# Kernel optimization log

Measured on AMD Instinct MI355X. Metric: run time of the kernel, lower is better.

The kernel has to match this reference:

```python
import jax, jax.numpy as jnp
import numpy as np

G, N, C_IN, C_OUT, HEADS = 64, 2048, 64, 64, 2
E = 1_000_000
T = G * N  # total flattened nodes
NEG_SLOPE = 0.2  # PyG GATv2Conv default


def setup_inputs() -> dict:
    key = jax.random.key(0)
    k_x, k_e, k_wl, k_wr, k_a, k_b = jax.random.split(key, 6)
    x = jax.random.normal(k_x, (G, N, C_IN), dtype=jnp.float32)
    edge_index = jax.random.randint(k_e, (2, E), 0, T, dtype=jnp.int64)
    # GATv2Conv params (share_weights=False): separate lin_l / lin_r, per-head att vector, bias
    s = 1.0 / np.sqrt(C_IN)
    W_l = jax.random.uniform(k_wl, (C_IN, HEADS * C_OUT), minval=-s, maxval=s, dtype=jnp.float32)
    W_r = jax.random.uniform(k_wr, (C_IN, HEADS * C_OUT), minval=-s, maxval=s, dtype=jnp.float32)
    att = jax.random.normal(k_a, (HEADS, C_OUT), dtype=jnp.float32) * 0.1
    bias = jax.random.normal(k_b, (HEADS * C_OUT,), dtype=jnp.float32) * 0.01
    return {"x": x, "edge_index": edge_index, "W_l": W_l, "W_r": W_r, "att": att, "bias": bias}


def reference(x, edge_index, W_l, W_r, att, bias):
    # Flatten batched nodes: (G, N, C_in) -> (T, C_in)
    x_flat = x.reshape(-1, C_IN)
    # Linear projections per side, split heads: (T, H, C)
    xl = (x_flat @ W_l).reshape(T, HEADS, C_OUT)
    xr = (x_flat @ W_r).reshape(T, HEADS, C_OUT)
    # add_self_loops=True: append (i, i) for every flattened node
    loop = jnp.arange(T, dtype=edge_index.dtype)
    src = jnp.concatenate([edge_index[0], loop])
    dst = jnp.concatenate([edge_index[1], loop])
    # GATv2 scoring: e_ij = att . LeakyReLU(xl[j] + xr[i])  -> (E', H)
    h = jax.nn.leaky_relu(xl[src] + xr[dst], negative_slope=NEG_SLOPE)
    score = jnp.einsum('ehc,hc->eh', h, att)
    # Segment softmax over incoming edges of each destination node
    m = jax.ops.segment_max(score, dst, num_segments=T)  # (T, H)
    ealpha = jnp.exp(score - m[dst])
    denom = jax.ops.segment_sum(ealpha, dst, num_segments=T)
    alpha = ealpha / denom[dst]  # self-loops guarantee denom > 0
    # Scatter-aggregate messages: out[i] = sum_j alpha_ij * xl[j]
    out = jax.ops.segment_sum(alpha[:, :, None] * xl[src], dst, num_segments=T)  # (T, H, C)
    out = out.reshape(T, HEADS * C_OUT) + bias
    return out.reshape(G, N, HEADS * C_OUT)
```

## Files before the change

### kernel.cpp

```cpp
#include <hip/hip_runtime.h>
#include <hip/hip_bf16.h>

#define T_NODES (64 * 2048)
#define CIN 64
#define HC 128
#define NEG_SLOPE 0.2f
#define GEMM_BLOCKS (T_NODES / 64)

typedef unsigned short ushort_t;
typedef __attribute__((ext_vector_type(8))) short bf16x8;
typedef __attribute__((ext_vector_type(4))) float f32x4;

__device__ __forceinline__ ushort_t f2bf(float x) {
    unsigned u = __float_as_uint(x);
    u += 0x7fffu + ((u >> 16) & 1u);
    return (ushort_t)(u >> 16);
}
__device__ __forceinline__ float bf2f(ushort_t b) {
    return __uint_as_float(((unsigned)b) << 16);
}

__global__ void prep_w(const float* __restrict__ Wl, const float* __restrict__ Wr,
                       uint4* __restrict__ wt) {
    const int t = blockIdx.x * 256 + threadIdx.x;
    const int n = t & 255, cc = t >> 8;
    const float* Wsrc = ((n < HC) ? Wl : Wr) + (n & (HC - 1));
    union { ushort_t u[8]; uint4 v; } pk;
#pragma unroll
    for (int j = 0; j < 8; ++j) pk.u[j] = f2bf(Wsrc[(cc * 8 + j) * HC]);
    const int sw = (n & 7) << 4;
    *(uint4*)((char*)wt + n * 128 + ((cc * 16) ^ sw)) = pk.v;
}

__global__ __launch_bounds__(256) void gemm_hist(const float* __restrict__ x,
                                                 const uint4* __restrict__ wt,
                                                 ushort_t* __restrict__ xl,
                                                 ushort_t* __restrict__ xr,
                                                 const int* __restrict__ ei,
                                                 unsigned* __restrict__ counts,
                                                 ushort_t* __restrict__ rank,
                                                 int E, int ET, int histBlocks) {
    __shared__ uint4 lds4[2560];
    const int tid = threadIdx.x;

    if (blockIdx.x < histBlocks) {
        const int b = blockIdx.x;
#pragma unroll
        for (int e = 0; e < 4; ++e) {
            int i = b * 1024 + e * 256 + tid;
            if (i < ET) {
                int dst = (i < E) ? ei[E + i] : (i - E);
                rank[i] = (ushort_t)atomicAdd(&counts[dst], 1u);
            }
        }
        return;
    }

    char* abase = (char*)lds4;
    char* wbase = (char*)lds4 + 8192;
    const int row0 = (blockIdx.x - histBlocks) * 64;

    {
        const int r = tid >> 2, c4 = tid & 3;
        const float4* xp = (const float4*)(x + (size_t)(row0 + r) * CIN + c4 * 16);
        float4 f0 = xp[0], f1 = xp[1], f2 = xp[2], f3 = xp[3];
        union { ushort_t u[16]; uint4 v[2]; } pk;
        const float s[16] = {f0.x,f0.y,f0.z,f0.w, f1.x,f1.y,f1.z,f1.w,
                             f2.x,f2.y,f2.z,f2.w, f3.x,f3.y,f3.z,f3.w};
#pragma unroll
        for (int j = 0; j < 16; ++j) pk.u[j] = f2bf(s[j]);
        const int sw = (r & 7) << 4;
        *(uint4*)(abase + r * 128 + ((c4 * 32)      ^ sw)) = pk.v[0];
        *(uint4*)(abase + r * 128 + ((c4 * 32 + 16) ^ sw)) = pk.v[1];
    }
    {
#pragma unroll
        for (int q = 0; q < 8; ++q)
            lds4[512 + q * 256 + tid] = wt[q * 256 + tid];
    }
    __syncthreads();

    const int wave = tid >> 6;
    const int lane = tid & 63;
    const int ar = lane & 15;
    const int kb = lane >> 4;

    bf16x8 afr[2][4], bfr[2][4];
#pragma unroll
    for (int kk = 0; kk < 2; ++kk) {
#pragma unroll
        for (int rt = 0; rt < 4; ++rt) {
            const int r = rt * 16 + ar;
            afr[kk][rt] = *(bf16x8*)(abase + r * 128 + ((kk * 64 + kb * 16) ^ ((r & 7) << 4)));
        }
#pragma unroll
        for (int ct = 0; ct < 4; ++ct) {
            const int n = wave * 64 + ct * 16 + ar;
            bfr[kk][ct] = *(bf16x8*)(wbase + n * 128 + ((kk * 64 + kb * 16) ^ ((n & 7) << 4)));
        }
    }

    f32x4 acc[4][4];
#pragma unroll
    for (int rt = 0; rt < 4; ++rt)
#pragma unroll
        for (int ct = 0; ct < 4; ++ct) acc[rt][ct] = (f32x4){0.f, 0.f, 0.f, 0.f};

#pragma unroll
    for (int kk = 0; kk < 2; ++kk)
#pragma unroll
        for (int rt = 0; rt < 4; ++rt)
#pragma unroll
            for (int ct = 0; ct < 4; ++ct)
                acc[rt][ct] = __builtin_amdgcn_mfma_f32_16x16x32_bf16(
                    afr[kk][rt], bfr[kk][ct], acc[rt][ct], 0, 0, 0);

    ushort_t* op = (wave < 2) ? xl : xr;
    const int colbase = (wave & 1) * 64 + ar;
    const int rowoff = (lane >> 4) * 4;
#pragma unroll
    for (int rt = 0; rt < 4; ++rt)
#pragma unroll
        for (int ct = 0; ct < 4; ++ct)
#pragma unroll
            for (int j = 0; j < 4; ++j)
                op[(size_t)(row0 + rt * 16 + rowoff + j) * HC + colbase + ct * 16] =
                    f2bf(acc[rt][ct][j]);
}

__global__ __launch_bounds__(256) void scan_tiles(const unsigned* __restrict__ counts,
                                                  unsigned* __restrict__ offs,
                                                  unsigned* __restrict__ partials) {
    __shared__ unsigned s[256];
    const int t = threadIdx.x;
    const int base = blockIdx.x * 1024 + t * 4;
    uint4 c = *(const uint4*)(counts + base);
    unsigned mysum = c.x + c.y + c.z + c.w;
    s[t] = mysum;
    __syncthreads();
    for (int off = 1; off < 256; off <<= 1) {
        unsigned v = (t >= off) ? s[t - off] : 0u;
        __syncthreads();
        s[t] += v;
        __syncthreads();
    }
    unsigned excl = s[t] - mysum;
    uint4 o;
    o.x = excl;
    o.y = excl + c.x;
    o.z = o.y + c.y;
    o.w = o.z + c.z;
    *(uint4*)(offs + base) = o;
    if (t == 255) partials[blockIdx.x] = s[255];
}

__global__ __launch_bounds__(256) void finalize_offs(unsigned* __restrict__ offs,
                                                     const unsigned* __restrict__ partials) {
    __shared__ unsigned s[128];
    const int t = threadIdx.x;
    const int tile = blockIdx.x >> 2;
    if (t < 128) s[t] = (t < tile) ? partials[t] : 0u;
    __syncthreads();
    for (int off = 64; off; off >>= 1) {
        if (t < off) s[t] += s[t + off];
        __syncthreads();
    }
    const unsigned base = s[0];
    const int i = blockIdx.x * 256 + t;
    offs[i] += base;
}

__global__ void scatter_edges(const int* __restrict__ ei,
                              const unsigned* __restrict__ offs,
                              const ushort_t* __restrict__ rank,
                              int* __restrict__ sorted_src, int E, int ET) {
    int i = blockIdx.x * 256 + threadIdx.x;
    if (i >= ET) return;
    int src, dst;
    if (i < E) { src = ei[i]; dst = ei[E + i]; }
    else       { src = dst = i - E; }
    sorted_src[offs[dst] + rank[i]] = src;
}

__global__ __launch_bounds__(256) void fused_aggr(const ushort_t* __restrict__ xl,
                                                  const ushort_t* __restrict__ xr,
                                                  const int* __restrict__ sorted_src,
                                                  const unsigned* __restrict__ offs,
                                                  const unsigned* __restrict__ counts,
                                                  const float* __restrict__ att,
                                                  const float* __restrict__ bias,
                                                  float* __restrict__ out) {
    const int tid = threadIdx.x;
    const int lane = tid & 63;
    int node = (blockIdx.x * 256 + tid) >> 6;
    node = __builtin_amdgcn_readfirstlane(node);
    const int slot = lane >> 4;
    const int sub  = lane & 15;
    const int cb   = sub * 8;

    float attv[8], xrv[8];
    {
        const float4 a0 = *(const float4*)(att + cb);
        const float4 a1 = *(const float4*)(att + cb + 4);
        attv[0]=a0.x; attv[1]=a0.y; attv[2]=a0.z; attv[3]=a0.w;
        attv[4]=a1.x; attv[5]=a1.y; attv[6]=a1.z; attv[7]=a1.w;
        const uint4 xv = *(const uint4*)(xr + (size_t)node * HC + cb);
        const ushort_t* xu = (const ushort_t*)&xv;
#pragma unroll
        for (int j = 0; j < 8; ++j) xrv[j] = bf2f(xu[j]);
    }

    const int start = (int)offs[node];
    const int cnt   = (int)counts[node];
    const int rounds = (cnt + 3) >> 2;

    float acc[8];
#pragma unroll
    for (int j = 0; j < 8; ++j) acc[j] = 0.f;
    float d = 0.f;

    for (int r = 0; r < rounds; ++r) {
        const int k = r * 4 + slot;
        const bool valid = k < cnt;
        const int src = sorted_src[start + (valid ? k : 0)];
        const uint4 v = *(const uint4*)(xl + (size_t)src * HC + cb);
        const ushort_t* vu = (const ushort_t*)&v;
        float a[8];
        float p = 0.f;
#pragma unroll
        for (int j = 0; j < 8; ++j) {
            a[j] = bf2f(vu[j]);
            float z = a[j] + xrv[j];
            float lr = z > 0.f ? z : NEG_SLOPE * z;
            p = __builtin_fmaf(attv[j], lr, p);
        }
        p += __shfl_xor(p, 1);
        p += __shfl_xor(p, 2);
        p += __shfl_xor(p, 4);
        const float e = valid ? __expf(p) : 0.f;
        d += e;
#pragma unroll
        for (int j = 0; j < 8; ++j) acc[j] = __builtin_fmaf(e, a[j], acc[j]);
    }

#pragma unroll
    for (int off = 16; off <= 32; off <<= 1) {
        d += __shfl_xor(d, off);
#pragma unroll
        for (int j = 0; j < 8; ++j) acc[j] += __shfl_xor(acc[j], off);
    }

    if (slot == 0) {
        const float inv = 1.f / d;
        const float4 b0 = *(const float4*)(bias + cb);
        const float4 b1 = *(const float4*)(bias + cb + 4);
        float4 o0, o1;
        o0.x = acc[0] * inv + b0.x; o0.y = acc[1] * inv + b0.y;
        o0.z = acc[2] * inv + b0.z; o0.w = acc[3] * inv + b0.w;
        o1.x = acc[4] * inv + b1.x; o1.y = acc[5] * inv + b1.y;
        o1.z = acc[6] * inv + b1.z; o1.w = acc[7] * inv + b1.w;
        float* op = out + (size_t)node * HC + cb;
        *(float4*)op = o0;
        *(float4*)(op + 4) = o1;
    }
}

extern "C" void kernel_launch(void* const* d_in, const int* in_sizes, int n_in,
                              void* d_out, int out_size, void* d_ws, size_t ws_size,
                              hipStream_t stream) {
    const float* x    = (const float*)d_in[0];
    const int*   ei   = (const int*)d_in[1];
    const float* Wl   = (const float*)d_in[2];
    const float* Wr   = (const float*)d_in[3];
    const float* att  = (const float*)d_in[4];
    const float* bias = (const float*)d_in[5];
    float* out = (float*)d_out;

    const int E  = in_sizes[1] / 2;
    const int ET = E + T_NODES;

    ushort_t* xl = (ushort_t*)d_ws;
    ushort_t* xr = xl + (size_t)T_NODES * HC;
    int* sorted_src = (int*)(xr + (size_t)T_NODES * HC);
    unsigned* counts   = (unsigned*)(sorted_src + ET);
    unsigned* offs     = counts + T_NODES;
    unsigned* partials = offs + T_NODES;
    ushort_t* rank     = (ushort_t*)(partials + 128);
    uint4* wt          = (uint4*)(rank + ((ET + 7) & ~7));

    hipMemsetAsync(counts, 0, (size_t)T_NODES * sizeof(unsigned), stream);

    prep_w<<<8, 256, 0, stream>>>(Wl, Wr, wt);

    const int histBlocks = (ET + 1023) / 1024;
    gemm_hist<<<histBlocks + GEMM_BLOCKS, 256, 0, stream>>>(x, wt, xl, xr,
                                                            ei, counts, rank,
                                                            E, ET, histBlocks);

    scan_tiles<<<T_NODES / 1024, 256, 0, stream>>>(counts, offs, partials);
    finalize_offs<<<T_NODES / 256, 256, 0, stream>>>(offs, partials);
    int eblocks = (ET + 255) / 256;
    scatter_edges<<<eblocks, 256, 0, stream>>>(ei, offs, rank, sorted_src, E, ET);

    fused_aggr<<<T_NODES / 4, 256, 0, stream>>>(xl, xr, sorted_src, offs, counts,
                                                att, bias, out);
}
```

Measured before the change: 163.7 us.

## Fuse memset into weight prep, single-pass decoupled scan, packed-float aggregation math

Replaces the hipMemsetAsync plus prep_w launch with one prep_init kernel that both converts the weights and zeroes the counts and partials. Merges scan_tiles and finalize_offs into a single scan_all kernel in which each block publishes its tile sum with a flag bit and spins on earlier tiles' flags to get its base offset. This removes two launches. In fused_aggr the per-channel math is rewritten with 2-wide float vectors, and byte-offset addressing is simplified, so the compiler can emit packed FP32 ops. The spin-wait scan relies on all 128 blocks being co-resident, and its correctness depends on the flag protocol.

```diff
diff --git a/kernel.cpp b/kernel.cpp
--- a/kernel.cpp
+++ b/kernel.cpp
@@ -10,6 +10,7 @@
 typedef unsigned short ushort_t;
 typedef __attribute__((ext_vector_type(8))) short bf16x8;
 typedef __attribute__((ext_vector_type(4))) float f32x4;
+typedef __attribute__((ext_vector_type(2))) float f32x2;
 
 __device__ __forceinline__ ushort_t f2bf(float x) {
     unsigned u = __float_as_uint(x);
@@ -19,17 +20,38 @@
 __device__ __forceinline__ float bf2f(ushort_t b) {
     return __uint_as_float(((unsigned)b) << 16);
 }
-
-__global__ void prep_w(const float* __restrict__ Wl, const float* __restrict__ Wr,
-                       uint4* __restrict__ wt) {
-    const int t = blockIdx.x * 256 + threadIdx.x;
-    const int n = t & 255, cc = t >> 8;
-    const float* Wsrc = ((n < HC) ? Wl : Wr) + (n & (HC - 1));
-    union { ushort_t u[8]; uint4 v; } pk;
-#pragma unroll
-    for (int j = 0; j < 8; ++j) pk.u[j] = f2bf(Wsrc[(cc * 8 + j) * HC]);
-    const int sw = (n & 7) << 4;
-    *(uint4*)((char*)wt + n * 128 + ((cc * 16) ^ sw)) = pk.v;
+__device__ __forceinline__ f32x2 bf2x2(unsigned w) {
+    f32x2 r;
+    r.x = __uint_as_float(w << 16);
+    r.y = __uint_as_float(w & 0xffff0000u);
+    return r;
+}
+__device__ __forceinline__ f32x2 pkmax(f32x2 a, f32x2 b) {
+    f32x2 r; r.x = fmaxf(a.x, b.x); r.y = fmaxf(a.y, b.y); return r;
+}
+
+__global__ __launch_bounds__(256) void prep_init(const float* __restrict__ Wl,
+                                                 const float* __restrict__ Wr,
+                                                 uint4* __restrict__ wt,
+                                                 unsigned* __restrict__ counts,
+                                                 unsigned* __restrict__ partials) {
+    const int bid = blockIdx.x, tid = threadIdx.x;
+    if (bid < 8) {
+        const int t = bid * 256 + tid;
+        const int n = t & 255, cc = t >> 8;
+        const float* Wsrc = ((n < HC) ? Wl : Wr) + (n & (HC - 1));
+        union { ushort_t u[8]; uint4 v; } pk;
+#pragma unroll
+        for (int j = 0; j < 8; ++j) pk.u[j] = f2bf(Wsrc[(cc * 8 + j) * HC]);
+        const int sw = (n & 7) << 4;
+        *(uint4*)((char*)wt + n * 128 + ((cc * 16) ^ sw)) = pk.v;
+        if (bid == 0 && tid < 128) partials[tid] = 0u;
+    } else {
+        const int i = (bid - 8) * 256 + tid;
+        uint4* c4 = (uint4*)counts;
+        c4[i * 2]     = (uint4){0, 0, 0, 0};
+        c4[i * 2 + 1] = (uint4){0, 0, 0, 0};
+    }
 }
 
 __global__ __launch_bounds__(256) void gemm_hist(const float* __restrict__ x,
@@ -128,13 +150,14 @@
                     f2bf(acc[rt][ct][j]);
 }
 
-__global__ __launch_bounds__(256) void scan_tiles(const unsigned* __restrict__ counts,
-                                                  unsigned* __restrict__ offs,
-                                                  unsigned* __restrict__ partials) {
+__global__ __launch_bounds__(256) void scan_all(const unsigned* __restrict__ counts,
+                                                unsigned* __restrict__ offs,
+                                                unsigned* __restrict__ partials) {
     __shared__ unsigned s[256];
-    const int t = threadIdx.x;
-    const int base = blockIdx.x * 1024 + t * 4;
-    uint4 c = *(const uint4*)(counts + base);
+    __shared__ unsigned wsum[4];
+    const int b = blockIdx.x, t = threadIdx.x;
+    const int base_i = b * 1024 + t * 4;
+    uint4 c = *(const uint4*)(counts + base_i);
     unsigned mysum = c.x + c.y + c.z + c.w;
     s[t] = mysum;
     __syncthreads();
@@ -144,30 +167,30 @@
         s[t] += v;
         __syncthreads();
     }
-    unsigned excl = s[t] - mysum;
+    const unsigned excl = s[t] - mysum;
+    if (t == 255)
+        __hip_atomic_store(&partials[b], s[255] | 0x80000000u,
+                           __ATOMIC_RELEASE, __HIP_MEMORY_SCOPE_AGENT);
+    unsigned bs = 0;
+    if (t < b) {
+        unsigned v;
+        do {
+            v = __hip_atomic_load(&partials[t], __ATOMIC_ACQUIRE,
+                                  __HIP_MEMORY_SCOPE_AGENT);
+        } while (!(v & 0x80000000u));
+        bs = v & 0x7fffffffu;
+    }
+#pragma unroll
+    for (int off = 32; off; off >>= 1) bs += __shfl_xor(bs, off);
+    if ((t & 63) == 0) wsum[t >> 6] = bs;
+    __syncthreads();
+    const unsigned base = wsum[0] + wsum[1] + wsum[2] + wsum[3];
     uint4 o;
-    o.x = excl;
-    o.y = excl + c.x;
+    o.x = excl + base;
+    o.y = o.x + c.x;
     o.z = o.y + c.y;
     o.w = o.z + c.z;
-    *(uint4*)(offs + base) = o;
-    if (t == 255) partials[blockIdx.x] = s[255];
-}
-
-__global__ __launch_bounds__(256) void finalize_offs(unsigned* __restrict__ offs,
-                                                     const unsigned* __restrict__ partials) {
-    __shared__ unsigned s[128];
-    const int t = threadIdx.x;
-    const int tile = blockIdx.x >> 2;
-    if (t < 128) s[t] = (t < tile) ? partials[t] : 0u;
-    __syncthreads();
-    for (int off = 64; off; off >>= 1) {
-        if (t < off) s[t] += s[t + off];
-        __syncthreads();
-    }
-    const unsigned base = s[0];
-    const int i = blockIdx.x * 256 + t;
-    offs[i] += base;
+    *(uint4*)(offs + base_i) = o;
 }
 
 __global__ void scatter_edges(const int* __restrict__ ei,
@@ -196,70 +219,73 @@
     node = __builtin_amdgcn_readfirstlane(node);
     const int slot = lane >> 4;
     const int sub  = lane & 15;
-    const int cb   = sub * 8;
-
-    float attv[8], xrv[8];
+    const unsigned cb2 = (unsigned)sub * 16u;
+
+    f32x2 attv[4], xrv[4];
     {
-        const float4 a0 = *(const float4*)(att + cb);
-        const float4 a1 = *(const float4*)(att + cb + 4);
-        attv[0]=a0.x; attv[1]=a0.y; attv[2]=a0.z; attv[3]=a0.w;
-        attv[4]=a1.x; attv[5]=a1.y; attv[6]=a1.z; attv[7]=a1.w;
-        const uint4 xv = *(const uint4*)(xr + (size_t)node * HC + cb);
-        const ushort_t* xu = (const ushort_t*)&xv;
-#pragma unroll
-        for (int j = 0; j < 8; ++j) xrv[j] = bf2f(xu[j]);
+        const f32x2* ap = (const f32x2*)(att + sub * 8);
+#pragma unroll
+        for (int q = 0; q < 4; ++q) attv[q] = ap[q];
+        const uint4 xv = *(const uint4*)((const char*)xr + (((unsigned)node << 8) + cb2));
+        const unsigned* xw = (const unsigned*)&xv;
+#pragma unroll
+        for (int q = 0; q < 4; ++q) xrv[q] = bf2x2(xw[q]);
     }
 
     const int start = (int)offs[node];
     const int cnt   = (int)counts[node];
     const int rounds = (cnt + 3) >> 2;
 
-    float acc[8];
-#pragma unroll
-    for (int j = 0; j < 8; ++j) acc[j] = 0.f;
+    f32x2 acc2[4];
+#pragma unroll
+    for (int q = 0; q < 4; ++q) acc2[q] = (f32x2){0.f, 0.f};
     float d = 0.f;
 
     for (int r = 0; r < rounds; ++r) {
         const int k = r * 4 + slot;
         const bool valid = k < cnt;
         const int src = sorted_src[start + (valid ? k : 0)];
-        const uint4 v = *(const uint4*)(xl + (size_t)src * HC + cb);
-        const ushort_t* vu = (const ushort_t*)&v;
-        float a[8];
-        float p = 0.f;
-#pragma unroll
-        for (int j = 0; j < 8; ++j) {
-            a[j] = bf2f(vu[j]);
-            float z = a[j] + xrv[j];
-            float lr = z > 0.f ? z : NEG_SLOPE * z;
-            p = __builtin_fmaf(attv[j], lr, p);
-        }
+        const uint4 v = *(const uint4*)((const char*)xl + (((unsigned)src << 8) + cb2));
+        const unsigned* vw = (const unsigned*)&v;
+        f32x2 a2[4];
+        f32x2 p2 = (f32x2){0.f, 0.f};
+#pragma unroll
+        for (int q = 0; q < 4; ++q) {
+            a2[q] = bf2x2(vw[q]);
+            f32x2 z = a2[q] + xrv[q];
+            z = pkmax(z, z * NEG_SLOPE);
+            p2 += attv[q] * z;
+        }
+        float p = p2.x + p2.y;
         p += __shfl_xor(p, 1);
         p += __shfl_xor(p, 2);
         p += __shfl_xor(p, 4);
         const float e = valid ? __expf(p) : 0.f;
         d += e;
-#pragma unroll
-        for (int j = 0; j < 8; ++j) acc[j] = __builtin_fmaf(e, a[j], acc[j]);
+        const f32x2 ev = (f32x2){e, e};
+#pragma unroll
+        for (int q = 0; q < 4; ++q) acc2[q] += ev * a2[q];
     }
 
 #pragma unroll
     for (int off = 16; off <= 32; off <<= 1) {
         d += __shfl_xor(d, off);
 #pragma unroll
-        for (int j = 0; j < 8; ++j) acc[j] += __shfl_xor(acc[j], off);
+        for (int q = 0; q < 4; ++q) {
+            acc2[q].x += __shfl_xor(acc2[q].x, off);
+            acc2[q].y += __shfl_xor(acc2[q].y, off);
+        }
     }
 
     if (slot == 0) {
         const float inv = 1.f / d;
-        const float4 b0 = *(const float4*)(bias + cb);
-        const float4 b1 = *(const float4*)(bias + cb + 4);
+        const f32x2* bp = (const f32x2*)(bias + sub * 8);
         float4 o0, o1;
-        o0.x = acc[0] * inv + b0.x; o0.y = acc[1] * inv + b0.y;
-        o0.z = acc[2] * inv + b0.z; o0.w = acc[3] * inv + b0.w;
-        o1.x = acc[4] * inv + b1.x; o1.y = acc[5] * inv + b1.y;
-        o1.z = acc[6] * inv + b1.z; o1.w = acc[7] * inv + b1.w;
-        float* op = out + (size_t)node * HC + cb;
+        o0.x = acc2[0].x * inv + bp[0].x; o0.y = acc2[0].y * inv + bp[0].y;
+        o0.z = acc2[1].x * inv + bp[1].x; o0.w = acc2[1].y * inv + bp[1].y;
+        o1.x = acc2[2].x * inv + bp[2].x; o1.y = acc2[2].y * inv + bp[2].y;
+        o1.z = acc2[3].x * inv + bp[3].x; o1.w = acc2[3].y * inv + bp[3].y;
+        float* op = out + (size_t)node * HC + sub * 8;
         *(float4*)op = o0;
         *(float4*)(op + 4) = o1;
     }
@@ -288,17 +314,14 @@
     ushort_t* rank     = (ushort_t*)(partials + 128);
     uint4* wt          = (uint4*)(rank + ((ET + 7) & ~7));
 
-    hipMemsetAsync(counts, 0, (size_t)T_NODES * sizeof(unsigned), stream);
-
-    prep_w<<<8, 256, 0, stream>>>(Wl, Wr, wt);
+    prep_init<<<72, 256, 0, stream>>>(Wl, Wr, wt, counts, partials);
 
     const int histBlocks = (ET + 1023) / 1024;
     gemm_hist<<<histBlocks + GEMM_BLOCKS, 256, 0, stream>>>(x, wt, xl, xr,
                                                             ei, counts, rank,
                                                             E, ET, histBlocks);
 
-    scan_tiles<<<T_NODES / 1024, 256, 0, stream>>>(counts, offs, partials);
-    finalize_offs<<<T_NODES / 256, 256, 0, stream>>>(offs, partials);
+    scan_all<<<T_NODES / 1024, 256, 0, stream>>>(counts, offs, partials);
     int eblocks = (ET + 255) / 256;
     scatter_edges<<<eblocks, 256, 0, stream>>>(ei, offs, rank, sorted_src, E, ET);
 
```

After: 165.1 us. No clear change (+0.8%).
